# Optimization experiments

Measured on AMD Instinct MI355X. Metric: run time of the kernel, lower is better.

## Reference

```python
import jax, jax.numpy as jnp
import numpy as np

NUM_HEADS = 16


def setup_inputs() -> dict:
    key = jax.random.key(0)
    ks = jax.random.split(key, 8)
    B, L, Hd = 2, 2048, 1024
    s = 0.02
    return {
        "x": jax.random.normal(ks[0], (B, L, Hd), jnp.float32),
        "y": jax.random.normal(ks[1], (B, L, Hd), jnp.float32),
        "mask": jnp.zeros((B, L), jnp.bool_),  # True = padding (masked out)
        "Wq_w": jax.random.normal(ks[2], (Hd, Hd), jnp.float32) * s,
        "Wq_b": jnp.zeros((Hd,), jnp.float32),
        "Wkv_w": jax.random.normal(ks[3], (Hd, 2 * Hd), jnp.float32) * s,
        "Wkv_b": jnp.zeros((2 * Hd,), jnp.float32),
        "proj_w": jax.random.normal(ks[4], (Hd, Hd), jnp.float32) * s,
        "proj_b": jnp.zeros((Hd,), jnp.float32),
    }


def reference(x, y, mask, Wq_w, Wq_b, Wkv_w, Wkv_b, proj_w, proj_b):
    B, L, Hd = x.shape
    H = NUM_HEADS
    D = Hd // H
    scale = 1.0 / np.sqrt(D)

    # projections (torch Linear: stored here already as (in, out))
    q = (x @ Wq_w + Wq_b).reshape(B, L, H, D).transpose(0, 2, 1, 3)   # bhld
    kv = (y @ Wkv_w + Wkv_b).reshape(B, L, 2, H, D)
    k = kv[:, :, 0].transpose(0, 2, 1, 3)                             # bhkd
    v = kv[:, :, 1].transpose(0, 2, 1, 3)                             # bhkd

    attn = jnp.einsum("bhld,bhkd->bhlk", q, k) * scale

    # combined padding (over keys) + causal mask; True = masked
    causal = jnp.triu(jnp.ones((L, L), jnp.bool_), 1)                 # (L, L)
    combined = mask[:, None, None, :] | causal[None, None]            # (B,1,L,L)
    attn = jnp.where(combined, -jnp.inf, attn)

    p = jax.nn.softmax(attn, axis=-1)
    out = jnp.einsum("bhlk,bhkd->bhld", p, v)
    out = out.transpose(0, 2, 1, 3).reshape(B, L, Hd)
    return out @ proj_w + proj_b
```

## Files before the change

### kernel.cpp

```cpp
#include <hip/hip_runtime.h>
#include <stdint.h>

#define B_  2
#define L_  2048
#define HD_ 1024
#define H_  16
#define D_  64

typedef unsigned short u16;
typedef __attribute__((ext_vector_type(8))) short bf16x8;
typedef __attribute__((ext_vector_type(4))) float f32x4;

#define MFMA16(a, b, c) __builtin_amdgcn_mfma_f32_16x16x32_bf16((a), (b), (c), 0, 0, 0)

__device__ __forceinline__ void gload16(const void* g, void* l) {
  __builtin_amdgcn_global_load_lds((const __attribute__((address_space(1))) void*)g,
                                   (__attribute__((address_space(3))) void*)l, 16, 0, 0);
}

__device__ __forceinline__ u16 f2bf(float f) {
  union { float f; uint32_t u; } c; c.f = f;
  uint32_t u = c.u + 0x7FFFu + ((c.u >> 16) & 1u);
  return (u16)(u >> 16);
}

__device__ __forceinline__ uint32_t cvt_pk_bf16(float lo, float hi) {
  uint32_t r;
  asm("v_cvt_pk_bf16_f32 %0, %1, %2" : "=v"(r) : "v"(lo), "v"(hi));
  return r;
}

__global__ void prologue_k(const float* __restrict__ x, const float* __restrict__ y,
                           u16* __restrict__ xb, u16* __restrict__ yb,
                           const float* __restrict__ Wq, const float* __restrict__ Wkv,
                           const float* __restrict__ Wp,
                           u16* __restrict__ Wqt, u16* __restrict__ Wkvt,
                           u16* __restrict__ Wpt) {
  int bid = blockIdx.x;
  int t = threadIdx.x;
  if (bid < 4096) {
    const float* in = bid < 2048 ? x : y;
    u16* out = bid < 2048 ? xb : yb;
    int i = ((bid & 2047) * 256 + t) * 8;
    float4 a = *(const float4*)(in + i);
    float4 b = *(const float4*)(in + i + 4);
    bf16x8 r;
    r[0] = (short)f2bf(a.x); r[1] = (short)f2bf(a.y); r[2] = (short)f2bf(a.z); r[3] = (short)f2bf(a.w);
    r[4] = (short)f2bf(b.x); r[5] = (short)f2bf(b.y); r[6] = (short)f2bf(b.z); r[7] = (short)f2bf(b.w);
    *(bf16x8*)(out + i) = r;
    return;
  }
  int f = bid - 4096;
  const float* src; u16* dst; int Nfull, bx, by;
  if (f < 1024)      { src = Wq;  dst = Wqt;  Nfull = 1024; bx = f & 31;  by = f >> 5; }
  else if (f < 3072) { int g2 = f - 1024; src = Wkv; dst = Wkvt; Nfull = 2048; bx = g2 & 63; by = g2 >> 6; }
  else               { int g2 = f - 3072; src = Wp;  dst = Wpt;  Nfull = 1024; bx = g2 & 31; by = g2 >> 5; }
  __shared__ float tile[32][33];
  int tc = t & 31, tr = t >> 5;
  int nb = bx * 32, kb = by * 32;
#pragma unroll
  for (int i = 0; i < 4; i++)
    tile[tr + i * 8][tc] = src[(size_t)(kb + tr + i * 8) * Nfull + nb + tc];
  __syncthreads();
#pragma unroll
  for (int i = 0; i < 4; i++) {
    int nl = tr + i * 8;
    dst[(size_t)(nb + nl) * 1024 + kb + tc] = f2bf(tile[tc][nl]);
  }
}

__device__ __forceinline__ void gemm_body(
    char* sA, char* sB,
    const u16* __restrict__ A, const u16* __restrict__ Bt,
    const float* __restrict__ bias, void* __restrict__ outp,
    int N, int epi, int bm, int bn)
{
  int t = threadIdx.x;
  int lane = t & 63, w = t >> 6;
  int g = lane >> 4, l15 = lane & 15;
  int wr = w >> 1, wc = w & 1;

  f32x4 zero = {0.f, 0.f, 0.f, 0.f};
  f32x4 acc[4][4];
#pragma unroll
  for (int mi = 0; mi < 4; mi++)
#pragma unroll
    for (int ni = 0; ni < 4; ni++) acc[mi][ni] = zero;

#define GSTAGE(bufi, k0s) do {                                                          \
    _Pragma("unroll")                                                                   \
    for (int it = 0; it < 4; it++) {                                                    \
      int c = it * 256 + t;                          \
      int r = c >> 3, sp = c & 7;                                                       \
      int off = (sp ^ (r & 7)) << 4;               \
      gload16((const char*)(A + (size_t)(bm + r) * 1024 + (k0s)) + off,                 \
              sA + (bufi) * 16384 + c * 16);                                            \
      gload16((const char*)(Bt + (size_t)(bn + r) * 1024 + (k0s)) + off,                \
              sB + (bufi) * 16384 + c * 16);                                            \
    } } while (0)

  GSTAGE(0, 0);
  int buf = 0;
#pragma unroll 1
  for (int kt = 0; kt < 16; kt++) {
    __builtin_amdgcn_sched_barrier(0);
    __builtin_amdgcn_s_barrier();
    if (kt < 15) {
      GSTAGE(buf ^ 1, (kt + 1) << 6);
      asm volatile("s_waitcnt vmcnt(8)" ::: "memory");
    } else {
      asm volatile("s_waitcnt vmcnt(0)" ::: "memory");
    }
    __builtin_amdgcn_s_barrier();
    __builtin_amdgcn_sched_barrier(0);

    const char* cA = sA + buf * 16384;
    const char* cB = sB + buf * 16384;
#pragma unroll
    for (int kc = 0; kc < 2; kc++) {
      bf16x8 af[4], bfr[4];
#pragma unroll
      for (int mi = 0; mi < 4; mi++) {
        int r = wr * 64 + mi * 16 + l15;
        af[mi] = *(const bf16x8*)(cA + r * 128 + (((kc * 4 + g) ^ (r & 7)) << 4));
      }
#pragma unroll
      for (int ni = 0; ni < 4; ni++) {
        int r = wc * 64 + ni * 16 + l15;
        bfr[ni] = *(const bf16x8*)(cB + r * 128 + (((kc * 4 + g) ^ (r & 7)) << 4));
      }
#pragma unroll
      for (int mi = 0; mi < 4; mi++)
#pragma unroll
        for (int ni = 0; ni < 4; ni++)
          acc[mi][ni] = MFMA16(af[mi], bfr[ni], acc[mi][ni]);
    }
    buf ^= 1;
  }
#undef GSTAGE

  float bv[4];
#pragma unroll
  for (int ni = 0; ni < 4; ni++) bv[ni] = bias[bn + wc * 64 + ni * 16 + l15];

  if (epi == 2) {
    float* fo = (float*)outp;
#pragma unroll
    for (int mi = 0; mi < 4; mi++)
#pragma unroll
      for (int ni = 0; ni < 4; ni++) {
        int n = bn + wc * 64 + ni * 16 + l15;
#pragma unroll
        for (int r = 0; r < 4; r++) {
          int m = bm + wr * 64 + mi * 16 + g * 4 + r;
          fo[(size_t)m * N + n] = acc[mi][ni][r] + bv[ni];
        }
      }
  } else {
    u16* ob = (u16*)outp;
#pragma unroll
    for (int mi = 0; mi < 4; mi++)
#pragma unroll
      for (int ni = 0; ni < 4; ni++) {
        int n = bn + wc * 64 + ni * 16 + l15;
        int kv = n >> 10;
        int hh = (n >> 6) & 15;
        int dd = n & 63;
        int m0 = bm + wr * 64 + mi * 16 + g * 4;
        int bb = m0 >> 11, lq0 = m0 & 2047;
        if (epi == 1 && kv == 1) {
          ushort4 pk;
          pk.x = f2bf(acc[mi][ni][0] + bv[ni]);
          pk.y = f2bf(acc[mi][ni][1] + bv[ni]);
          pk.z = f2bf(acc[mi][ni][2] + bv[ni]);
          pk.w = f2bf(acc[mi][ni][3] + bv[ni]);
          size_t idx = (size_t)(B_ * H_ * L_ * D_) +
                       (((size_t)(bb * H_ + hh) * D_ + dd) * L_ + lq0);
          *(ushort4*)(ob + idx) = pk;
        } else {
#pragma unroll
          for (int r = 0; r < 4; r++) {
            size_t idx = (((size_t)(bb * H_ + hh) * L_ + lq0 + r) * D_) + dd;
            ob[idx] = f2bf(acc[mi][ni][r] + bv[ni]);
          }
        }
      }
  }
}

__global__ __launch_bounds__(256) void qkv_k(
    const u16* __restrict__ xb, const u16* __restrict__ yb,
    const u16* __restrict__ Wqt, const u16* __restrict__ Wkvt,
    const float* __restrict__ Wq_b, const float* __restrict__ Wkv_b,
    u16* __restrict__ Qout, u16* __restrict__ KVout)
{
  __shared__ char sA[2 * 16384];
  __shared__ char sB[2 * 16384];
  int bx = blockIdx.x, by = blockIdx.y;
  if (by < 16) {
    gemm_body(sA, sB, yb, Wkvt, Wkv_b, (void*)KVout, 2048, 1, by * 128, bx * 128);
    __syncthreads();
    gemm_body(sA, sB, yb, Wkvt, Wkv_b, (void*)KVout, 2048, 1, (by + 16) * 128, bx * 128);
  } else {
    gemm_body(sA, sB, xb, Wqt, Wq_b, (void*)Qout, 1024, 0,
              (2 * (by - 16) + (bx >> 3)) * 128, (bx & 7) * 128);
  }
}

__global__ __launch_bounds__(256) void gemm_k(
    const u16* __restrict__ A, const u16* __restrict__ Bt,
    const float* __restrict__ bias, void* __restrict__ outp, int N)
{
  __shared__ char sA[2 * 16384];
  __shared__ char sB[2 * 16384];
  gemm_body(sA, sB, A, Bt, bias, outp, N, 2, blockIdx.y * 128, blockIdx.x * 128);
}

__global__ __launch_bounds__(512, 2) void attn_k(
    const u16* __restrict__ Qb, const u16* __restrict__ Kb, const u16* __restrict__ Vt,
    const unsigned char* __restrict__ pad, u16* __restrict__ Ob)
{
  __shared__ char sK[3][8192];
  __shared__ char sV[3][8192];
  __shared__ char sP[8][2048];
  int t = threadIdx.x, lane = t & 63, w = t >> 6, g = lane >> 4, l15 = lane & 15;
  int x = blockIdx.x, h = blockIdx.y, b = blockIdx.z, bh = b * H_ + h;
  int qb = b ? x : 15 - x;

  const u16* Kbh = Kb + (size_t)bh * L_ * D_;
  const u16* Vbh = Vt + (size_t)bh * D_ * L_;
  const unsigned char* pdb = pad + b * L_;
  const float SCL = 0.125f * 1.44269504089f;
  int psw = l15 & 7;

  int srr = t >> 3, ssp = t & 7;
  int sso = (ssp ^ (srr & 7)) << 4;
#define STAGE(bufi, kt0s) do {                                                        \
    gload16((const char*)(Kbh + (size_t)((kt0s) + srr) * D_) + sso, sK[bufi] + t * 16); \
    gload16((const char*)(Vbh + (size_t)srr * L_ + (kt0s)) + sso, sV[bufi] + t * 16);   \
  } while (0)

  int qw0 = qb * 128 + w * 16;
  int bound = qw0 + 15;
  int nkt = 2 * qb + 2;

  const u16* qp = Qb + ((size_t)bh * L_ + qw0 + l15) * D_ + g * 8;
  bf16x8 qf0 = *(const bf16x8*)qp;
  bf16x8 qf1 = *(const bf16x8*)(qp + 32);

  f32x4 zero = {0.f, 0.f, 0.f, 0.f};
  f32x4 oacc[4];
#pragma unroll
  for (int db = 0; db < 4; db++) oacc[db] = zero;
  float mrun = -1e30f, lrun = 0.f;

  STAGE(0, 0);
  int cb = 0, nb = 1;

#pragma unroll 1
  for (int kt = 0; kt < nkt; kt++) {
    int kt0 = kt << 6;
    __builtin_amdgcn_sched_barrier(0);
    if (kt + 1 < nkt) {
      STAGE(nb, (kt + 1) << 6);
      asm volatile("s_waitcnt vmcnt(2)" ::: "memory");
    } else {
      asm volatile("s_waitcnt vmcnt(0)" ::: "memory");
    }
    __builtin_amdgcn_s_barrier();
    __builtin_amdgcn_sched_barrier(0);

    if (kt0 <= bound) {
      float sc[4][4];
#pragma unroll
      for (int s = 0; s < 4; s++) {
        int kb = kt0 + s * 16;
        bool live = (kb <= bound);
        f32x4 st = zero;
        uint32_t pb = 0;
        if (live) {
          int R = s * 16 + l15, sw = l15 & 7;
          bf16x8 kf0 = *(const bf16x8*)(sK[cb] + R * 128 + ((g ^ sw) << 4));
          bf16x8 kf1 = *(const bf16x8*)(sK[cb] + R * 128 + (((4 + g) ^ sw) << 4));
          __builtin_amdgcn_s_setprio(1);
          st = MFMA16(kf0, qf0, st);
          st = MFMA16(kf1, qf1, st);
          __builtin_amdgcn_s_setprio(0);
          pb = *(const uint32_t*)(pdb + kb + 4 * g);
        }
        bool needm = !live || (kb + 15 > qw0) || (__ballot(pb != 0) != 0);
        if (needm) {
#pragma unroll
          for (int r = 0; r < 4; r++) {
            int key = kb + 4 * g + r;
            bool pm = (pb >> (8 * r)) & 0xffu;
            bool msk = !live || pm || (key > qw0 + l15);
            sc[s][r] = msk ? -1e30f : st[r] * SCL;
          }
        } else {
#pragma unroll
          for (int r = 0; r < 4; r++) sc[s][r] = st[r] * SCL;
        }
      }

      float m0 = fmaxf(fmaxf(sc[0][0], sc[0][1]), fmaxf(sc[0][2], sc[0][3]));
      float m1 = fmaxf(fmaxf(sc[1][0], sc[1][1]), fmaxf(sc[1][2], sc[1][3]));
      float m2 = fmaxf(fmaxf(sc[2][0], sc[2][1]), fmaxf(sc[2][2], sc[2][3]));
      float m3 = fmaxf(fmaxf(sc[3][0], sc[3][1]), fmaxf(sc[3][2], sc[3][3]));
      float mt = fmaxf(fmaxf(m0, m1), fmaxf(m2, m3));
      mt = fmaxf(mt, __shfl_xor(mt, 16));
      mt = fmaxf(mt, __shfl_xor(mt, 32));
      if (!__all(mt <= mrun)) {
        float mnew = fmaxf(mrun, mt);
        float al = __builtin_amdgcn_exp2f(mrun - mnew);
        mrun = mnew;
        lrun *= al;
#pragma unroll
        for (int db = 0; db < 4; db++)
#pragma unroll
          for (int r = 0; r < 4; r++) oacc[db][r] *= al;
      }
      float rs = 0.f;
      char* pwb = sP[w] + l15 * 128 + (g & 1) * 8;
#pragma unroll
      for (int s = 0; s < 4; s++) {
        float p0 = __builtin_amdgcn_exp2f(sc[s][0] - mrun);
        float p1 = __builtin_amdgcn_exp2f(sc[s][1] - mrun);
        float p2 = __builtin_amdgcn_exp2f(sc[s][2] - mrun);
        float p3 = __builtin_amdgcn_exp2f(sc[s][3] - mrun);
        rs += (p0 + p1) + (p2 + p3);
        uint32_t w0 = cvt_pk_bf16(p0, p1), w1 = cvt_pk_bf16(p2, p3);
        char* dst = pwb + (((2 * s + (g >> 1)) ^ psw) << 4);
        *(uint32_t*)dst = w0;
        *(uint32_t*)(dst + 4) = w1;
      }
      rs += __shfl_xor(rs, 16);
      rs += __shfl_xor(rs, 32);
      lrun += rs;

#pragma unroll
      for (int kc = 0; kc < 2; kc++) {
        if (kt0 + 32 * kc <= bound) {
          bf16x8 pf = *(const bf16x8*)(sP[w] + l15 * 128 + (((4 * kc + g) ^ psw) << 4));
          __builtin_amdgcn_s_setprio(1);
#pragma unroll
          for (int db = 0; db < 4; db++) {
            int dR = db * 16 + l15;
            bf16x8 vf = *(const bf16x8*)(sV[cb] + dR * 128 +
                                         (((4 * kc + g) ^ (dR & 7)) << 4));
            oacc[db] = MFMA16(vf, pf, oacc[db]);
          }
          __builtin_amdgcn_s_setprio(0);
        }
      }
    }
    cb = (cb == 2) ? 0 : cb + 1;
    nb = (nb == 2) ? 0 : nb + 1;
  }

  float rl = 1.0f / lrun;
  int q = qw0 + l15;
  u16* op = Ob + ((size_t)b * L_ + q) * HD_ + h * D_ + g * 4;
#pragma unroll
  for (int db = 0; db < 4; db++) {
    ushort4 pk;
    pk.x = f2bf(oacc[db][0] * rl);
    pk.y = f2bf(oacc[db][1] * rl);
    pk.z = f2bf(oacc[db][2] * rl);
    pk.w = f2bf(oacc[db][3] * rl);
    *(ushort4*)(op + db * 16) = pk;
  }
#undef STAGE
}

extern "C" void kernel_launch(void* const* d_in, const int* in_sizes, int n_in,
                              void* d_out, int out_size, void* d_ws, size_t ws_size,
                              hipStream_t stream) {
  const float* x      = (const float*)d_in[0];
  const float* y      = (const float*)d_in[1];
  const unsigned char* mask = (const unsigned char*)d_in[2];
  const float* Wq_w   = (const float*)d_in[3];
  const float* Wq_b   = (const float*)d_in[4];
  const float* Wkv_w  = (const float*)d_in[5];
  const float* Wkv_b  = (const float*)d_in[6];
  const float* proj_w = (const float*)d_in[7];
  const float* proj_b = (const float*)d_in[8];

  char* ws = (char*)d_ws;
  u16* xb   = (u16*)(ws);
  u16* yb   = (u16*)(ws + (size_t)(8  << 20));
  u16* Wqt  = (u16*)(ws + (size_t)(16 << 20));
  u16* Wkvt = (u16*)(ws + (size_t)(18 << 20));
  u16* Wpt  = (u16*)(ws + (size_t)(22 << 20));
  u16* Qb   = (u16*)(ws + (size_t)(24 << 20));
  u16* Kb   = (u16*)(ws + (size_t)(32 << 20));
  u16* Vtb  = (u16*)(ws + (size_t)(40 << 20));
  u16* Ob   = xb;

  hipLaunchKernelGGL(prologue_k, dim3(8192), dim3(256), 0, stream,
                     x, y, xb, yb, Wq_w, Wkv_w, proj_w, Wqt, Wkvt, Wpt);
  hipLaunchKernelGGL(qkv_k, dim3(16, 32), dim3(256), 0, stream,
                     xb, yb, Wqt, Wkvt, Wq_b, Wkv_b, Qb, Kb);
  hipLaunchKernelGGL(attn_k, dim3(16, H_, B_), dim3(512), 0, stream, Qb, Kb, Vtb, mask, Ob);
  hipLaunchKernelGGL(gemm_k, dim3(8, 32), dim3(256), 0, stream, Ob, Wpt, proj_b, d_out, 1024);
}
```

Baseline: 134.9 us.

## Use 128-key attention tiles with double-buffered K/V staging

The attention kernel now processes 128 keys per iteration instead of 64, so it runs half as many loop iterations. K/V staging moves from a triple buffer of 64-key tiles to a double buffer of 128-key tiles, with an extra barrier at the top of each iteration before the next tile is loaded. The V layout changes to 256-byte rows with a 16-way XOR swizzle. Fewer barriers and waits per key are meant to reduce overhead and improve MFMA density. In exchange, more registers are live (sc[8][4]), there is more causal-masking waste on the diagonal tile, and the loads can overlap with compute less.

```diff
diff --git a/kernel.cpp b/kernel.cpp
--- a/kernel.cpp
+++ b/kernel.cpp
@@ -220,8 +220,8 @@
     const u16* __restrict__ Qb, const u16* __restrict__ Kb, const u16* __restrict__ Vt,
     const unsigned char* __restrict__ pad, u16* __restrict__ Ob)
 {
-  __shared__ char sK[3][8192];
-  __shared__ char sV[3][8192];
+  __shared__ char sK[2][16384];
+  __shared__ char sV[2][16384];
   __shared__ char sP[8][2048];
   int t = threadIdx.x, lane = t & 63, w = t >> 6, g = lane >> 4, l15 = lane & 15;
   int x = blockIdx.x, h = blockIdx.y, b = blockIdx.z, bh = b * H_ + h;
@@ -233,16 +233,21 @@
   const float SCL = 0.125f * 1.44269504089f;
   int psw = l15 & 7;
 
-  int srr = t >> 3, ssp = t & 7;
-  int sso = (ssp ^ (srr & 7)) << 4;
-#define STAGE(bufi, kt0s) do {                                                        \
-    gload16((const char*)(Kbh + (size_t)((kt0s) + srr) * D_) + sso, sK[bufi] + t * 16); \
-    gload16((const char*)(Vbh + (size_t)srr * L_ + (kt0s)) + sso, sV[bufi] + t * 16);   \
-  } while (0)
+#define STAGE(bufi, kt0s) do {                                                          \
+    _Pragma("unroll")                                                                   \
+    for (int ii = 0; ii < 2; ii++) {                                                    \
+      int cc = ii * 512 + t;                                                            \
+      int kr = cc >> 3, ks = cc & 7;                                                    \
+      gload16((const char*)(Kbh + (size_t)((kt0s) + kr) * D_) + ((ks ^ (kr & 7)) << 4), \
+              sK[bufi] + cc * 16);                                                      \
+      int vr = cc >> 4, vs = cc & 15;                                                   \
+      gload16((const char*)(Vbh + (size_t)vr * L_ + (kt0s) + ((vs ^ (vr & 15)) << 3)),  \
+              sV[bufi] + cc * 16);                                                      \
+    } } while (0)
 
   int qw0 = qb * 128 + w * 16;
   int bound = qw0 + 15;
-  int nkt = 2 * qb + 2;
+  int nkt = qb + 1;
 
   const u16* qp = Qb + ((size_t)bh * L_ + qw0 + l15) * D_ + g * 8;
   bf16x8 qf0 = *(const bf16x8*)qp;
@@ -255,107 +260,109 @@
   float mrun = -1e30f, lrun = 0.f;
 
   STAGE(0, 0);
-  int cb = 0, nb = 1;
+  int buf = 0;
 
 #pragma unroll 1
   for (int kt = 0; kt < nkt; kt++) {
-    int kt0 = kt << 6;
+    int kt0 = kt << 7;
     __builtin_amdgcn_sched_barrier(0);
+    __builtin_amdgcn_s_barrier();
     if (kt + 1 < nkt) {
-      STAGE(nb, (kt + 1) << 6);
-      asm volatile("s_waitcnt vmcnt(2)" ::: "memory");
+      STAGE(buf ^ 1, (kt + 1) << 7);
+      asm volatile("s_waitcnt vmcnt(4)" ::: "memory");
     } else {
       asm volatile("s_waitcnt vmcnt(0)" ::: "memory");
     }
     __builtin_amdgcn_s_barrier();
     __builtin_amdgcn_sched_barrier(0);
 
-    if (kt0 <= bound) {
-      float sc[4][4];
-#pragma unroll
-      for (int s = 0; s < 4; s++) {
-        int kb = kt0 + s * 16;
-        bool live = (kb <= bound);
-        f32x4 st = zero;
-        uint32_t pb = 0;
-        if (live) {
-          int R = s * 16 + l15, sw = l15 & 7;
-          bf16x8 kf0 = *(const bf16x8*)(sK[cb] + R * 128 + ((g ^ sw) << 4));
-          bf16x8 kf1 = *(const bf16x8*)(sK[cb] + R * 128 + (((4 + g) ^ sw) << 4));
-          __builtin_amdgcn_s_setprio(1);
-          st = MFMA16(kf0, qf0, st);
-          st = MFMA16(kf1, qf1, st);
-          __builtin_amdgcn_s_setprio(0);
-          pb = *(const uint32_t*)(pdb + kb + 4 * g);
+    float sc[8][4];
+#pragma unroll
+    for (int s = 0; s < 8; s++) {
+      int kb = kt0 + s * 16;
+      bool live = (kb <= bound);
+      f32x4 st = zero;
+      uint32_t pb = 0;
+      if (live) {
+        int R = s * 16 + l15, sw = R & 7;
+        bf16x8 kf0 = *(const bf16x8*)(sK[buf] + R * 128 + ((g ^ sw) << 4));
+        bf16x8 kf1 = *(const bf16x8*)(sK[buf] + R * 128 + (((4 + g) ^ sw) << 4));
+        st = MFMA16(kf0, qf0, st);
+        st = MFMA16(kf1, qf1, st);
+        pb = *(const uint32_t*)(pdb + kb + 4 * g);
+      }
+      bool needm = !live || (kb + 15 > qw0) || (__ballot(pb != 0) != 0);
+      if (needm) {
+#pragma unroll
+        for (int r = 0; r < 4; r++) {
+          int key = kb + 4 * g + r;
+          bool pm = (pb >> (8 * r)) & 0xffu;
+          bool msk = !live || pm || (key > qw0 + l15);
+          sc[s][r] = msk ? -1e30f : st[r] * SCL;
         }
-        bool needm = !live || (kb + 15 > qw0) || (__ballot(pb != 0) != 0);
-        if (needm) {
-#pragma unroll
-          for (int r = 0; r < 4; r++) {
-            int key = kb + 4 * g + r;
-            bool pm = (pb >> (8 * r)) & 0xffu;
-            bool msk = !live || pm || (key > qw0 + l15);
-            sc[s][r] = msk ? -1e30f : st[r] * SCL;
+      } else {
+#pragma unroll
+        for (int r = 0; r < 4; r++) sc[s][r] = st[r] * SCL;
+      }
+    }
+
+    float ms[8];
+#pragma unroll
+    for (int s = 0; s < 8; s++)
+      ms[s] = fmaxf(fmaxf(sc[s][0], sc[s][1]), fmaxf(sc[s][2], sc[s][3]));
+    float mt = fmaxf(fmaxf(fmaxf(ms[0], ms[1]), fmaxf(ms[2], ms[3])),
+                     fmaxf(fmaxf(ms[4], ms[5]), fmaxf(ms[6], ms[7])));
+    mt = fmaxf(mt, __shfl_xor(mt, 16));
+    mt = fmaxf(mt, __shfl_xor(mt, 32));
+    if (!__all(mt <= mrun)) {
+      float mnew = fmaxf(mrun, mt);
+      float al = __builtin_amdgcn_exp2f(mrun - mnew);
+      mrun = mnew;
+      lrun *= al;
+#pragma unroll
+      for (int db = 0; db < 4; db++)
+#pragma unroll
+        for (int r = 0; r < 4; r++) oacc[db][r] *= al;
+    }
+
+    float rs = 0.f;
+    char* pwb = sP[w] + l15 * 128 + (g & 1) * 8;
+#pragma unroll
+    for (int hh = 0; hh < 2; hh++) {
+      if (kt0 + hh * 64 <= bound) {
+#pragma unroll
+        for (int s2 = 0; s2 < 4; s2++) {
+          int s = 4 * hh + s2;
+          float p0 = __builtin_amdgcn_exp2f(sc[s][0] - mrun);
+          float p1 = __builtin_amdgcn_exp2f(sc[s][1] - mrun);
+          float p2 = __builtin_amdgcn_exp2f(sc[s][2] - mrun);
+          float p3 = __builtin_amdgcn_exp2f(sc[s][3] - mrun);
+          rs += (p0 + p1) + (p2 + p3);
+          uint32_t w0 = cvt_pk_bf16(p0, p1), w1 = cvt_pk_bf16(p2, p3);
+          char* dst = pwb + (((2 * s2 + (g >> 1)) ^ psw) << 4);
+          *(uint32_t*)dst = w0;
+          *(uint32_t*)(dst + 4) = w1;
+        }
+#pragma unroll
+        for (int kc = 0; kc < 2; kc++) {
+          if (kt0 + hh * 64 + 32 * kc <= bound) {
+            bf16x8 pf = *(const bf16x8*)(sP[w] + l15 * 128 + (((4 * kc + g) ^ psw) << 4));
+            int vslot = hh * 8 + kc * 4 + g;
+#pragma unroll
+            for (int db = 0; db < 4; db++) {
+              int dR = db * 16 + l15;
+              bf16x8 vf = *(const bf16x8*)(sV[buf] + dR * 256 +
+                                           ((vslot ^ (dR & 15)) << 4));
+              oacc[db] = MFMA16(vf, pf, oacc[db]);
+            }
           }
-        } else {
-#pragma unroll
-          for (int r = 0; r < 4; r++) sc[s][r] = st[r] * SCL;
         }
       }
-
-      float m0 = fmaxf(fmaxf(sc[0][0], sc[0][1]), fmaxf(sc[0][2], sc[0][3]));
-      float m1 = fmaxf(fmaxf(sc[1][0], sc[1][1]), fmaxf(sc[1][2], sc[1][3]));
-      float m2 = fmaxf(fmaxf(sc[2][0], sc[2][1]), fmaxf(sc[2][2], sc[2][3]));
-      float m3 = fmaxf(fmaxf(sc[3][0], sc[3][1]), fmaxf(sc[3][2], sc[3][3]));
-      float mt = fmaxf(fmaxf(m0, m1), fmaxf(m2, m3));
-      mt = fmaxf(mt, __shfl_xor(mt, 16));
-      mt = fmaxf(mt, __shfl_xor(mt, 32));
-      if (!__all(mt <= mrun)) {
-        float mnew = fmaxf(mrun, mt);
-        float al = __builtin_amdgcn_exp2f(mrun - mnew);
-        mrun = mnew;
-        lrun *= al;
-#pragma unroll
-        for (int db = 0; db < 4; db++)
-#pragma unroll
-          for (int r = 0; r < 4; r++) oacc[db][r] *= al;
-      }
-      float rs = 0.f;
-      char* pwb = sP[w] + l15 * 128 + (g & 1) * 8;
-#pragma unroll
-      for (int s = 0; s < 4; s++) {
-        float p0 = __builtin_amdgcn_exp2f(sc[s][0] - mrun);
-        float p1 = __builtin_amdgcn_exp2f(sc[s][1] - mrun);
-        float p2 = __builtin_amdgcn_exp2f(sc[s][2] - mrun);
-        float p3 = __builtin_amdgcn_exp2f(sc[s][3] - mrun);
-        rs += (p0 + p1) + (p2 + p3);
-        uint32_t w0 = cvt_pk_bf16(p0, p1), w1 = cvt_pk_bf16(p2, p3);
-        char* dst = pwb + (((2 * s + (g >> 1)) ^ psw) << 4);
-        *(uint32_t*)dst = w0;
-        *(uint32_t*)(dst + 4) = w1;
-      }
-      rs += __shfl_xor(rs, 16);
-      rs += __shfl_xor(rs, 32);
-      lrun += rs;
-
-#pragma unroll
-      for (int kc = 0; kc < 2; kc++) {
-        if (kt0 + 32 * kc <= bound) {
-          bf16x8 pf = *(const bf16x8*)(sP[w] + l15 * 128 + (((4 * kc + g) ^ psw) << 4));
-          __builtin_amdgcn_s_setprio(1);
-#pragma unroll
-          for (int db = 0; db < 4; db++) {
-            int dR = db * 16 + l15;
-            bf16x8 vf = *(const bf16x8*)(sV[cb] + dR * 128 +
-                                         (((4 * kc + g) ^ (dR & 7)) << 4));
-            oacc[db] = MFMA16(vf, pf, oacc[db]);
-          }
-          __builtin_amdgcn_s_setprio(0);
-        }
-      }
-    }
-    cb = (cb == 2) ? 0 : cb + 1;
-    nb = (nb == 2) ? 0 : nb + 1;
+    }
+    rs += __shfl_xor(rs, 16);
+    rs += __shfl_xor(rs, 32);
+    lrun += rs;
+    buf ^= 1;
   }
 
   float rl = 1.0f / lrun;
```

Result: no change. 133.2 us (-1.2%).

## Split long causal query blocks across workgroups and merge partial softmax results

Applied to the files above, without the earlier changes.

The attention kernel now gives each workgroup an even share of key tiles. Half the workgroups process the first 17 key tiles of a high query block. The other half fully process a low query block and then the remaining tiles of the matching high query block. Each half writes its partial output plus running max and sum to scratch buffers, and a new merge kernel combines them with log-sum-exp weights. The aim is to remove the causal load imbalance where the longest workgroup sets the kernel time. The cost is an extra launch, extra global traffic, and bf16 rounding of the partial outputs. The setprio hints around the MFMAs are also removed.

```diff
diff --git a/kernel.cpp b/kernel.cpp
--- a/kernel.cpp
+++ b/kernel.cpp
@@ -22,6 +22,11 @@
   union { float f; uint32_t u; } c; c.f = f;
   uint32_t u = c.u + 0x7FFFu + ((c.u >> 16) & 1u);
   return (u16)(u >> 16);
+}
+
+__device__ __forceinline__ float bf2f(u16 v) {
+  union { uint32_t u; float f; } c; c.u = (uint32_t)v << 16;
+  return c.f;
 }
 
 __device__ __forceinline__ uint32_t cvt_pk_bf16(float lo, float hi) {
@@ -218,14 +223,18 @@
 
 __global__ __launch_bounds__(512, 2) void attn_k(
     const u16* __restrict__ Qb, const u16* __restrict__ Kb, const u16* __restrict__ Vt,
-    const unsigned char* __restrict__ pad, u16* __restrict__ Ob)
+    const unsigned char* __restrict__ pad, u16* __restrict__ Ob,
+    u16* __restrict__ Opart, float* __restrict__ mlbuf)
 {
   __shared__ char sK[3][8192];
   __shared__ char sV[3][8192];
   __shared__ char sP[8][2048];
   int t = threadIdx.x, lane = t & 63, w = t >> 6, g = lane >> 4, l15 = lane & 15;
   int x = blockIdx.x, h = blockIdx.y, b = blockIdx.z, bh = b * H_ + h;
-  int qb = b ? x : 15 - x;
+  int role = x >> 3, xp = x & 7;
+  int qbH = 15 - xp, qbL = xp;
+  int nktH = 2 * qbH + 2;
+  const int SPLIT = 17;
 
   const u16* Kbh = Kb + (size_t)bh * L_ * D_;
   const u16* Vbh = Vt + (size_t)bh * D_ * L_;
@@ -240,137 +249,185 @@
     gload16((const char*)(Vbh + (size_t)srr * L_ + (kt0s)) + sso, sV[bufi] + t * 16);   \
   } while (0)
 
-  int qw0 = qb * 128 + w * 16;
-  int bound = qw0 + 15;
-  int nkt = 2 * qb + 2;
-
-  const u16* qp = Qb + ((size_t)bh * L_ + qw0 + l15) * D_ + g * 8;
-  bf16x8 qf0 = *(const bf16x8*)qp;
-  bf16x8 qf1 = *(const bf16x8*)(qp + 32);
-
-  f32x4 zero = {0.f, 0.f, 0.f, 0.f};
-  f32x4 oacc[4];
-#pragma unroll
-  for (int db = 0; db < 4; db++) oacc[db] = zero;
-  float mrun = -1e30f, lrun = 0.f;
-
-  STAGE(0, 0);
-  int cb = 0, nb = 1;
-
+  int nphase = role ? 1 : 2;
 #pragma unroll 1
-  for (int kt = 0; kt < nkt; kt++) {
-    int kt0 = kt << 6;
-    __builtin_amdgcn_sched_barrier(0);
-    if (kt + 1 < nkt) {
-      STAGE(nb, (kt + 1) << 6);
-      asm volatile("s_waitcnt vmcnt(2)" ::: "memory");
+  for (int ph = 0; ph < nphase; ph++) {
+    int qb, lo, hi, mode;
+    if (role) { qb = qbH; lo = 0;     hi = SPLIT;     mode = 1; }
+    else if (ph == 0) { qb = qbL; lo = 0; hi = 2 * qbL + 2; mode = 0; }
+    else { qb = qbH; lo = SPLIT; hi = nktH; mode = 2; }
+
+    int qw0 = qb * 128 + w * 16;
+    int bound = qw0 + 15;
+
+    const u16* qp = Qb + ((size_t)bh * L_ + qw0 + l15) * D_ + g * 8;
+    bf16x8 qf0 = *(const bf16x8*)qp;
+    bf16x8 qf1 = *(const bf16x8*)(qp + 32);
+
+    f32x4 zero = {0.f, 0.f, 0.f, 0.f};
+    f32x4 oacc[4];
+#pragma unroll
+    for (int db = 0; db < 4; db++) oacc[db] = zero;
+    float mrun = -1e30f, lrun = 0.f;
+
+    if (ph) __syncthreads();
+    STAGE(0, lo << 6);
+    int cb = 0, nb = 1;
+
+#pragma unroll 1
+    for (int kt = lo; kt < hi; kt++) {
+      int kt0 = kt << 6;
+      __builtin_amdgcn_sched_barrier(0);
+      if (kt + 1 < hi) {
+        STAGE(nb, (kt + 1) << 6);
+        asm volatile("s_waitcnt vmcnt(2)" ::: "memory");
+      } else {
+        asm volatile("s_waitcnt vmcnt(0)" ::: "memory");
+      }
+      __builtin_amdgcn_s_barrier();
+      __builtin_amdgcn_sched_barrier(0);
+
+      if (kt0 <= bound) {
+        float sc[4][4];
+#pragma unroll
+        for (int s = 0; s < 4; s++) {
+          int kb = kt0 + s * 16;
+          bool live = (kb <= bound);
+          f32x4 st = zero;
+          uint32_t pb = 0;
+          if (live) {
+            int R = s * 16 + l15, sw = l15 & 7;
+            bf16x8 kf0 = *(const bf16x8*)(sK[cb] + R * 128 + ((g ^ sw) << 4));
+            bf16x8 kf1 = *(const bf16x8*)(sK[cb] + R * 128 + (((4 + g) ^ sw) << 4));
+            st = MFMA16(kf0, qf0, st);
+            st = MFMA16(kf1, qf1, st);
+            pb = *(const uint32_t*)(pdb + kb + 4 * g);
+          }
+          bool needm = !live || (kb + 15 > qw0) || (__ballot(pb != 0) != 0);
+          if (needm) {
+#pragma unroll
+            for (int r = 0; r < 4; r++) {
+              int key = kb + 4 * g + r;
+              bool pm = (pb >> (8 * r)) & 0xffu;
+              bool msk = !live || pm || (key > qw0 + l15);
+              sc[s][r] = msk ? -1e30f : st[r] * SCL;
+            }
+          } else {
+#pragma unroll
+            for (int r = 0; r < 4; r++) sc[s][r] = st[r] * SCL;
+          }
+        }
+
+        float m0 = fmaxf(fmaxf(sc[0][0], sc[0][1]), fmaxf(sc[0][2], sc[0][3]));
+        float m1 = fmaxf(fmaxf(sc[1][0], sc[1][1]), fmaxf(sc[1][2], sc[1][3]));
+        float m2 = fmaxf(fmaxf(sc[2][0], sc[2][1]), fmaxf(sc[2][2], sc[2][3]));
+        float m3 = fmaxf(fmaxf(sc[3][0], sc[3][1]), fmaxf(sc[3][2], sc[3][3]));
+        float mt = fmaxf(fmaxf(m0, m1), fmaxf(m2, m3));
+        mt = fmaxf(mt, __shfl_xor(mt, 16));
+        mt = fmaxf(mt, __shfl_xor(mt, 32));
+        if (!__all(mt <= mrun)) {
+          float mnew = fmaxf(mrun, mt);
+          float al = __builtin_amdgcn_exp2f(mrun - mnew);
+          mrun = mnew;
+          lrun *= al;
+#pragma unroll
+          for (int db = 0; db < 4; db++)
+#pragma unroll
+            for (int r = 0; r < 4; r++) oacc[db][r] *= al;
+        }
+        float rs = 0.f;
+        char* pwb = sP[w] + l15 * 128 + (g & 1) * 8;
+#pragma unroll
+        for (int s = 0; s < 4; s++) {
+          float p0 = __builtin_amdgcn_exp2f(sc[s][0] - mrun);
+          float p1 = __builtin_amdgcn_exp2f(sc[s][1] - mrun);
+          float p2 = __builtin_amdgcn_exp2f(sc[s][2] - mrun);
+          float p3 = __builtin_amdgcn_exp2f(sc[s][3] - mrun);
+          rs += (p0 + p1) + (p2 + p3);
+          uint32_t w0 = cvt_pk_bf16(p0, p1), w1 = cvt_pk_bf16(p2, p3);
+          char* dst = pwb + (((2 * s + (g >> 1)) ^ psw) << 4);
+          *(uint32_t*)dst = w0;
+          *(uint32_t*)(dst + 4) = w1;
+        }
+        rs += __shfl_xor(rs, 16);
+        rs += __shfl_xor(rs, 32);
+        lrun += rs;
+
+#pragma unroll
+        for (int kc = 0; kc < 2; kc++) {
+          if (kt0 + 32 * kc <= bound) {
+            bf16x8 pf = *(const bf16x8*)(sP[w] + l15 * 128 + (((4 * kc + g) ^ psw) << 4));
+#pragma unroll
+            for (int db = 0; db < 4; db++) {
+              int dR = db * 16 + l15;
+              bf16x8 vf = *(const bf16x8*)(sV[cb] + dR * 128 +
+                                           (((4 * kc + g) ^ (dR & 7)) << 4));
+              oacc[db] = MFMA16(vf, pf, oacc[db]);
+            }
+          }
+        }
+      }
+      cb = (cb == 2) ? 0 : cb + 1;
+      nb = (nb == 2) ? 0 : nb + 1;
+    }
+
+    float rl = (lrun != 0.f) ? 1.0f / lrun : 0.f;
+    int q = qw0 + l15;
+    if (mode == 0) {
+      u16* op = Ob + ((size_t)b * L_ + q) * HD_ + h * D_ + g * 4;
+#pragma unroll
+      for (int db = 0; db < 4; db++) {
+        ushort4 pk;
+        pk.x = f2bf(oacc[db][0] * rl);
+        pk.y = f2bf(oacc[db][1] * rl);
+        pk.z = f2bf(oacc[db][2] * rl);
+        pk.w = f2bf(oacc[db][3] * rl);
+        *(ushort4*)(op + db * 16) = pk;
+      }
     } else {
-      asm volatile("s_waitcnt vmcnt(0)" ::: "memory");
+      int part = mode - 1;
+      size_t prow = (size_t)part * 32768 + (size_t)bh * 1024 + (q - 1024);
+      u16* op = Opart + prow * 64 + g * 4;
+#pragma unroll
+      for (int db = 0; db < 4; db++) {
+        ushort4 pk;
+        pk.x = f2bf(oacc[db][0] * rl);
+        pk.y = f2bf(oacc[db][1] * rl);
+        pk.z = f2bf(oacc[db][2] * rl);
+        pk.w = f2bf(oacc[db][3] * rl);
+        *(ushort4*)(op + db * 16) = pk;
+      }
+      if (g == 0) {
+        mlbuf[prow * 2]     = mrun;
+        mlbuf[prow * 2 + 1] = lrun;
+      }
     }
-    __builtin_amdgcn_s_barrier();
-    __builtin_amdgcn_sched_barrier(0);
-
-    if (kt0 <= bound) {
-      float sc[4][4];
-#pragma unroll
-      for (int s = 0; s < 4; s++) {
-        int kb = kt0 + s * 16;
-        bool live = (kb <= bound);
-        f32x4 st = zero;
-        uint32_t pb = 0;
-        if (live) {
-          int R = s * 16 + l15, sw = l15 & 7;
-          bf16x8 kf0 = *(const bf16x8*)(sK[cb] + R * 128 + ((g ^ sw) << 4));
-          bf16x8 kf1 = *(const bf16x8*)(sK[cb] + R * 128 + (((4 + g) ^ sw) << 4));
-          __builtin_amdgcn_s_setprio(1);
-          st = MFMA16(kf0, qf0, st);
-          st = MFMA16(kf1, qf1, st);
-          __builtin_amdgcn_s_setprio(0);
-          pb = *(const uint32_t*)(pdb + kb + 4 * g);
-        }
-        bool needm = !live || (kb + 15 > qw0) || (__ballot(pb != 0) != 0);
-        if (needm) {
-#pragma unroll
-          for (int r = 0; r < 4; r++) {
-            int key = kb + 4 * g + r;
-            bool pm = (pb >> (8 * r)) & 0xffu;
-            bool msk = !live || pm || (key > qw0 + l15);
-            sc[s][r] = msk ? -1e30f : st[r] * SCL;
-          }
-        } else {
-#pragma unroll
-          for (int r = 0; r < 4; r++) sc[s][r] = st[r] * SCL;
-        }
-      }
-
-      float m0 = fmaxf(fmaxf(sc[0][0], sc[0][1]), fmaxf(sc[0][2], sc[0][3]));
-      float m1 = fmaxf(fmaxf(sc[1][0], sc[1][1]), fmaxf(sc[1][2], sc[1][3]));
-      float m2 = fmaxf(fmaxf(sc[2][0], sc[2][1]), fmaxf(sc[2][2], sc[2][3]));
-      float m3 = fmaxf(fmaxf(sc[3][0], sc[3][1]), fmaxf(sc[3][2], sc[3][3]));
-      float mt = fmaxf(fmaxf(m0, m1), fmaxf(m2, m3));
-      mt = fmaxf(mt, __shfl_xor(mt, 16));
-      mt = fmaxf(mt, __shfl_xor(mt, 32));
-      if (!__all(mt <= mrun)) {
-        float mnew = fmaxf(mrun, mt);
-        float al = __builtin_amdgcn_exp2f(mrun - mnew);
-        mrun = mnew;
-        lrun *= al;
-#pragma unroll
-        for (int db = 0; db < 4; db++)
-#pragma unroll
-          for (int r = 0; r < 4; r++) oacc[db][r] *= al;
-      }
-      float rs = 0.f;
-      char* pwb = sP[w] + l15 * 128 + (g & 1) * 8;
-#pragma unroll
-      for (int s = 0; s < 4; s++) {
-        float p0 = __builtin_amdgcn_exp2f(sc[s][0] - mrun);
-        float p1 = __builtin_amdgcn_exp2f(sc[s][1] - mrun);
-        float p2 = __builtin_amdgcn_exp2f(sc[s][2] - mrun);
-        float p3 = __builtin_amdgcn_exp2f(sc[s][3] - mrun);
-        rs += (p0 + p1) + (p2 + p3);
-        uint32_t w0 = cvt_pk_bf16(p0, p1), w1 = cvt_pk_bf16(p2, p3);
-        char* dst = pwb + (((2 * s + (g >> 1)) ^ psw) << 4);
-        *(uint32_t*)dst = w0;
-        *(uint32_t*)(dst + 4) = w1;
-      }
-      rs += __shfl_xor(rs, 16);
-      rs += __shfl_xor(rs, 32);
-      lrun += rs;
-
-#pragma unroll
-      for (int kc = 0; kc < 2; kc++) {
-        if (kt0 + 32 * kc <= bound) {
-          bf16x8 pf = *(const bf16x8*)(sP[w] + l15 * 128 + (((4 * kc + g) ^ psw) << 4));
-          __builtin_amdgcn_s_setprio(1);
-#pragma unroll
-          for (int db = 0; db < 4; db++) {
-            int dR = db * 16 + l15;
-            bf16x8 vf = *(const bf16x8*)(sV[cb] + dR * 128 +
-                                         (((4 * kc + g) ^ (dR & 7)) << 4));
-            oacc[db] = MFMA16(vf, pf, oacc[db]);
-          }
-          __builtin_amdgcn_s_setprio(0);
-        }
-      }
-    }
-    cb = (cb == 2) ? 0 : cb + 1;
-    nb = (nb == 2) ? 0 : nb + 1;
-  }
-
-  float rl = 1.0f / lrun;
-  int q = qw0 + l15;
-  u16* op = Ob + ((size_t)b * L_ + q) * HD_ + h * D_ + g * 4;
-#pragma unroll
-  for (int db = 0; db < 4; db++) {
-    ushort4 pk;
-    pk.x = f2bf(oacc[db][0] * rl);
-    pk.y = f2bf(oacc[db][1] * rl);
-    pk.z = f2bf(oacc[db][2] * rl);
-    pk.w = f2bf(oacc[db][3] * rl);
-    *(ushort4*)(op + db * 16) = pk;
   }
 #undef STAGE
+}
+
+__global__ __launch_bounds__(256) void merge_k(
+    const u16* __restrict__ Op, const float* __restrict__ ml, u16* __restrict__ Ob)
+{
+  int tid = blockIdx.x * 256 + threadIdx.x;
+  int d0 = (tid & 7) * 8;
+  int row = tid >> 3;
+  int qrel = row & 1023, bh = row >> 10;
+  int b = bh >> 4, h = bh & 15;
+  float m0 = ml[(size_t)row * 2],            l0 = ml[(size_t)row * 2 + 1];
+  float m1 = ml[((size_t)32768 + row) * 2],  l1 = ml[((size_t)32768 + row) * 2 + 1];
+  float M = fmaxf(m0, m1);
+  float w0 = l0 * __builtin_amdgcn_exp2f(m0 - M);
+  float w1 = l1 * __builtin_amdgcn_exp2f(m1 - M);
+  float rw = 1.0f / (w0 + w1);
+  w0 *= rw; w1 *= rw;
+  bf16x8 a = *(const bf16x8*)(Op + (size_t)row * 64 + d0);
+  bf16x8 c = *(const bf16x8*)(Op + ((size_t)32768 + row) * 64 + d0);
+  bf16x8 o;
+#pragma unroll
+  for (int j = 0; j < 8; j++)
+    o[j] = (short)f2bf(w0 * bf2f((u16)a[j]) + w1 * bf2f((u16)c[j]));
+  *(bf16x8*)(Ob + ((size_t)b * L_ + 1024 + qrel) * HD_ + h * D_ + d0) = o;
 }
 
 extern "C" void kernel_launch(void* const* d_in, const int* in_sizes, int n_in,
@@ -396,11 +453,15 @@
   u16* Kb   = (u16*)(ws + (size_t)(32 << 20));
   u16* Vtb  = (u16*)(ws + (size_t)(40 << 20));
   u16* Ob   = xb;
+  u16* Opart  = yb;
+  float* mlbuf = (float*)Wqt;
 
   hipLaunchKernelGGL(prologue_k, dim3(8192), dim3(256), 0, stream,
                      x, y, xb, yb, Wq_w, Wkv_w, proj_w, Wqt, Wkvt, Wpt);
   hipLaunchKernelGGL(qkv_k, dim3(16, 32), dim3(256), 0, stream,
                      xb, yb, Wqt, Wkvt, Wq_b, Wkv_b, Qb, Kb);
-  hipLaunchKernelGGL(attn_k, dim3(16, H_, B_), dim3(512), 0, stream, Qb, Kb, Vtb, mask, Ob);
+  hipLaunchKernelGGL(attn_k, dim3(16, H_, B_), dim3(512), 0, stream,
+                     Qb, Kb, Vtb, mask, Ob, Opart, mlbuf);
+  hipLaunchKernelGGL(merge_k, dim3(1024), dim3(256), 0, stream, Opart, mlbuf, Ob);
   hipLaunchKernelGGL(gemm_k, dim3(8, 32), dim3(256), 0, stream, Ob, Wpt, proj_b, d_out, 1024);
 }
```

Result: faster. 125.8 us (-6.7%).
